# Kernel optimization log

Measured on AMD Instinct MI355X. Metric: run time of the kernel, lower is better.

Reference implementation:

```python
import math
import jax, jax.numpy as jnp
import numpy as np

IN_F, OUT_F = 2048, 2048
WINDOW = 64
SPARSE_RATIO = 0.1


def make_block_mask(in_f, out_f, window, ratio, seed=0):
    # Faithful reimplementation of RandomLinear mask construction.
    p0, p1 = min(in_f, out_f), max(in_f, out_f)
    d = math.ceil(p1 / p0)
    x = math.ceil(p0 / window)
    y = math.ceil((p1 // d) / window)
    blocks = x * y
    nnz = math.ceil(blocks * ratio)
    rng = np.random.default_rng(seed)
    ind = rng.permutation(blocks)[:nnz]
    m = np.zeros((p0, p1), np.float32)
    for k in range(nnz):
        bx = int(ind[k]) // y
        by = int(ind[k]) % y
        m[bx * window:(bx + 1) * window, by * window * d:(by + 1) * window * d] = 1.0
    if in_f <= out_f:
        m = m.T  # mask stored as [out_features, in_features]
    return jnp.asarray(m)


def setup_inputs() -> dict:
    key = jax.random.key(0)
    k_x, k_w, k_b = jax.random.split(key, 3)
    x = jax.random.normal(k_x, (4, 8192, IN_F), dtype=jnp.float32)
    mask = make_block_mask(IN_F, OUT_F, WINDOW, SPARSE_RATIO)
    # kaiming_uniform_(a=sqrt(5)) -> U(-bound, bound), bound = sqrt(6/((1+5)*fan_in)) = 1/sqrt(fan_in)
    bound_w = 1.0 / math.sqrt(IN_F)
    weight = jax.random.uniform(k_w, (OUT_F, IN_F), dtype=jnp.float32,
                                minval=-bound_w, maxval=bound_w)
    density = float(jnp.sum(mask)) / (IN_F * OUT_F)
    weight = weight / math.sqrt(density)  # rescale per reset_parameters
    bound_b = 1.0 / math.sqrt(IN_F)
    bias = jax.random.uniform(k_b, (OUT_F,), dtype=jnp.float32,
                              minval=-bound_b, maxval=bound_b)
    return {"input": x, "weight": weight, "mask": mask, "bias": bias}


def reference(input, weight, mask, bias):
    # y = x @ (mask * W)^T + b   ; x: [B,S,in], W/mask: [out,in], b: [out]
    w_eff = mask * weight
    return jnp.einsum('bsi,oi->bso', input, w_eff) + bias
```

## Files before the change

### kernel.cpp

```cpp
#include <hip/hip_runtime.h>

#define IN_F    2048
#define OUT_F   2048
#define BK      64
#define BM      256
#define BN      64
#define NKB     32
#define NOB     32
#define THREADS 256

__global__ __launch_bounds__(THREADS, 2)
void rl_sparse_fp32(const float* __restrict__ x,
                    const float* __restrict__ w,
                    const float* __restrict__ mask,
                    const float* __restrict__ bias,
                    float* __restrict__ out)
{
    __shared__ __align__(16) float xs[BM * BK];
    __shared__ __align__(16) float wsb[BN * BK];

    const int tid = threadIdx.x;
    const int ob  = blockIdx.x & (NOB - 1);
    const int mt  = blockIdx.x >> 5;
    const size_t m_base = (size_t)mt * BM;
    const int n_base = ob * BN;

    const int lane = tid & 63;
    float mv = 0.0f;
    if (lane < NKB)
        mv = mask[(size_t)n_base * IN_F + (size_t)lane * BK];
    unsigned long long kbits = __ballot(mv != 0.0f);

    const int tn = tid & 7;
    const int tm = tid >> 3;
    const int selx = tm & 3;
    const int selw = tn & 3;

    const int sc = tid & 15;
    const int sr = tid >> 4;

    float acc[8][8];
    #pragma unroll
    for (int i = 0; i < 8; ++i)
        #pragma unroll
        for (int j = 0; j < 8; ++j) acc[i][j] = 0.0f;

    while (kbits) {
        const int kb = __ffsll(kbits) - 1;
        kbits &= (kbits - 1);
        const size_t kcol = (size_t)kb * BK;

        const float* xg = x + m_base * IN_F + kcol + sc * 4;
        float4 vx[BM / 16];
        #pragma unroll
        for (int it = 0; it < BM / 16; ++it)
            vx[it] = *(const float4*)(xg + (size_t)(sr + 16 * it) * IN_F);

        const float* wg = w    + (size_t)(n_base + sr) * IN_F + kcol + sc * 4;
        const float* mg = mask + (size_t)(n_base + sr) * IN_F + kcol + sc * 4;
        float4 vw[BN / 16];
        #pragma unroll
        for (int it = 0; it < BN / 16; ++it) {
            float4 a = *(const float4*)(wg + (size_t)(16 * it) * IN_F);
            float4 b = *(const float4*)(mg + (size_t)(16 * it) * IN_F);
            a.x *= b.x; a.y *= b.y; a.z *= b.z; a.w *= b.w;
            vw[it] = a;
        }

        __syncthreads();

        #pragma unroll
        for (int it = 0; it < BM / 16; ++it) {
            const int r = sr + 16 * it;
            const int ch = sc ^ ((r >> 3) & 3);
            *(float4*)(&xs[r * BK + ch * 4]) = vx[it];
        }
        #pragma unroll
        for (int it = 0; it < BN / 16; ++it) {
            const int r = sr + 16 * it;
            const int ch = sc ^ ((r >> 3) & 3);
            *(float4*)(&wsb[r * BK + ch * 4]) = vw[it];
        }
        __syncthreads();

        const float* xrow = &xs[tm * 8 * BK];
        const float* wrow = &wsb[tn * 8 * BK];
        #pragma unroll 4
        for (int kc = 0; kc < 16; ++kc) {
            const int offx = ((kc ^ selx) << 2);
            const int offw = ((kc ^ selw) << 2);
            float4 xv[8], wv[8];
            #pragma unroll
            for (int i = 0; i < 8; ++i)
                xv[i] = *(const float4*)(xrow + i * BK + offx);
            #pragma unroll
            for (int j = 0; j < 8; ++j)
                wv[j] = *(const float4*)(wrow + j * BK + offw);
            #pragma unroll
            for (int i = 0; i < 8; ++i)
                #pragma unroll
                for (int j = 0; j < 8; ++j) {
                    acc[i][j] += xv[i].x * wv[j].x;
                    acc[i][j] += xv[i].y * wv[j].y;
                    acc[i][j] += xv[i].z * wv[j].z;
                    acc[i][j] += xv[i].w * wv[j].w;
                }
        }
    }

    const float4 b0 = *(const float4*)(bias + n_base + tn * 8);
    const float4 b1 = *(const float4*)(bias + n_base + tn * 8 + 4);
    #pragma unroll
    for (int i = 0; i < 8; ++i) {
        const size_t row = m_base + tm * 8 + i;
        float* op = out + row * OUT_F + n_base + tn * 8;
        float4 o0 = make_float4(acc[i][0] + b0.x, acc[i][1] + b0.y,
                                acc[i][2] + b0.z, acc[i][3] + b0.w);
        float4 o1 = make_float4(acc[i][4] + b1.x, acc[i][5] + b1.y,
                                acc[i][6] + b1.z, acc[i][7] + b1.w);
        *(float4*)(op)     = o0;
        *(float4*)(op + 4) = o1;
    }
}

extern "C" void kernel_launch(void* const* d_in, const int* in_sizes, int n_in,
                              void* d_out, int out_size, void* d_ws, size_t ws_size,
                              hipStream_t stream) {
    const float* x    = (const float*)d_in[0];
    const float* w    = (const float*)d_in[1];
    const float* mask = (const float*)d_in[2];
    const float* bias = (const float*)d_in[3];
    float* out = (float*)d_out;

    const int M = in_sizes[0] / IN_F;
    dim3 grid((M / BM) * NOB);
    rl_sparse_fp32<<<grid, THREADS, 0, stream>>>(x, w, mask, bias, out);
}
```

Before: 1.202 ms.

## Stream x tiles into LDS with global_load_lds and halve K-stage size

Splits each 64-wide K block into two 32-wide stages and loads x directly from global memory into LDS with the AMD global_load_lds builtin, using an XOR swizzle so no register staging is needed. Weight and mask loads for the next stage are prefetched into registers while the current stage computes. The smaller LDS footprint lets occupancy rise to three blocks per CU. The output column mapping changes to split columns into two 32-wide halves. The cost is twice as many barriers per K block and correctness that depends on the swizzle and on the direct-to-LDS write layout.

New measurement: 1.372 ms. +14.1%, slower.

```diff
diff --git a/kernel.cpp b/kernel.cpp
--- a/kernel.cpp
+++ b/kernel.cpp
@@ -2,22 +2,26 @@
 
 #define IN_F    2048
 #define OUT_F   2048
-#define BK      64
+#define BKW     64
+#define BSTAGE  32
 #define BM      256
 #define BN      64
 #define NKB     32
 #define NOB     32
 #define THREADS 256
 
-__global__ __launch_bounds__(THREADS, 2)
-void rl_sparse_fp32(const float* __restrict__ x,
-                    const float* __restrict__ w,
-                    const float* __restrict__ mask,
-                    const float* __restrict__ bias,
-                    float* __restrict__ out)
+typedef __attribute__((address_space(3))) void lds_void_t;
+typedef const __attribute__((address_space(1))) void gbl_void_t;
+
+__global__ __launch_bounds__(THREADS, 3)
+void rl_sparse_v2(const float* __restrict__ x,
+                  const float* __restrict__ w,
+                  const float* __restrict__ mask,
+                  const float* __restrict__ bias,
+                  float* __restrict__ out)
 {
-    __shared__ __align__(16) float xs[BM * BK];
-    __shared__ __align__(16) float wsb[BN * BK];
+    __shared__ __align__(16) float xs[BM * BSTAGE];
+    __shared__ __align__(16) float wsb[BN * BSTAGE];
 
     const int tid = threadIdx.x;
     const int ob  = blockIdx.x & (NOB - 1);
@@ -26,18 +30,19 @@
     const int n_base = ob * BN;
 
     const int lane = tid & 63;
-    float mv = 0.0f;
-    if (lane < NKB)
-        mv = mask[(size_t)n_base * IN_F + (size_t)lane * BK];
-    unsigned long long kbits = __ballot(mv != 0.0f);
+    float mvs = 0.0f;
+    if (lane < NKB) mvs = mask[(size_t)n_base * IN_F + (size_t)lane * BKW];
+    unsigned long long rem = __ballot(mvs != 0.0f);
 
     const int tn = tid & 7;
     const int tm = tid >> 3;
-    const int selx = tm & 3;
-    const int selw = tn & 3;
 
-    const int sc = tid & 15;
-    const int sr = tid >> 4;
+    const int gl_wave = tid >> 6;
+    const int gl_l    = tid & 63;
+
+    const int wrow = tid >> 2;
+    const int wc0  = tid & 3;
+    const int selw_st = (wrow >> 2) & 7;
 
     float acc[8][8];
     #pragma unroll
@@ -45,57 +50,77 @@
         #pragma unroll
         for (int j = 0; j < 8; ++j) acc[i][j] = 0.0f;
 
-    while (kbits) {
-        const int kb = __ffsll(kbits) - 1;
-        kbits &= (kbits - 1);
-        const size_t kcol = (size_t)kb * BK;
+    int cur_kb = rem ? (__ffsll(rem) - 1) : -1;
+    int cur_half = 0;
 
-        const float* xg = x + m_base * IN_F + kcol + sc * 4;
-        float4 vx[BM / 16];
-        #pragma unroll
-        for (int it = 0; it < BM / 16; ++it)
-            vx[it] = *(const float4*)(xg + (size_t)(sr + 16 * it) * IN_F);
+    float4 wra, wrb, mra, mrb;
+    if (cur_kb >= 0) {
+        const size_t kc0 = (size_t)cur_kb * BKW;
+        const float* wp = w    + (size_t)(n_base + wrow) * IN_F + kc0;
+        const float* mp = mask + (size_t)(n_base + wrow) * IN_F + kc0;
+        wra = *(const float4*)(wp + wc0 * 4);
+        wrb = *(const float4*)(wp + (wc0 + 4) * 4);
+        mra = *(const float4*)(mp + wc0 * 4);
+        mrb = *(const float4*)(mp + (wc0 + 4) * 4);
+    }
 
-        const float* wg = w    + (size_t)(n_base + sr) * IN_F + kcol + sc * 4;
-        const float* mg = mask + (size_t)(n_base + sr) * IN_F + kcol + sc * 4;
-        float4 vw[BN / 16];
-        #pragma unroll
-        for (int it = 0; it < BN / 16; ++it) {
-            float4 a = *(const float4*)(wg + (size_t)(16 * it) * IN_F);
-            float4 b = *(const float4*)(mg + (size_t)(16 * it) * IN_F);
-            a.x *= b.x; a.y *= b.y; a.z *= b.z; a.w *= b.w;
-            vw[it] = a;
+    while (cur_kb >= 0) {
+        const size_t kcol = (size_t)cur_kb * BKW + (size_t)cur_half * BSTAGE;
+
+        unsigned long long nrem = rem;
+        int nxt_kb = cur_kb, nxt_half = cur_half + 1;
+        if (nxt_half == 2) {
+            nrem &= (nrem - 1);
+            nxt_half = 0;
+            nxt_kb = nrem ? (__ffsll(nrem) - 1) : -1;
         }
 
         __syncthreads();
 
         #pragma unroll
-        for (int it = 0; it < BM / 16; ++it) {
-            const int r = sr + 16 * it;
-            const int ch = sc ^ ((r >> 3) & 3);
-            *(float4*)(&xs[r * BK + ch * 4]) = vx[it];
+        for (int I = 0; I < 8; ++I) {
+            const int row = gl_wave * 64 + I * 8 + (gl_l >> 3);
+            const int cch = (gl_l & 7) ^ I;
+            const float* src = x + (m_base + row) * (size_t)IN_F + kcol + cch * 4;
+            __builtin_amdgcn_global_load_lds((gbl_void_t*)src,
+                                             (lds_void_t*)&xs[(gl_wave * 64 + I * 8) * BSTAGE],
+                                             16, 0, 0);
         }
-        #pragma unroll
-        for (int it = 0; it < BN / 16; ++it) {
-            const int r = sr + 16 * it;
-            const int ch = sc ^ ((r >> 3) & 3);
-            *(float4*)(&wsb[r * BK + ch * 4]) = vw[it];
+
+        float4 va, vb;
+        va.x = wra.x * mra.x; va.y = wra.y * mra.y; va.z = wra.z * mra.z; va.w = wra.w * mra.w;
+        vb.x = wrb.x * mrb.x; vb.y = wrb.y * mrb.y; vb.z = wrb.z * mrb.z; vb.w = wrb.w * mrb.w;
+
+        if (nxt_kb >= 0) {
+            const size_t nk = (size_t)nxt_kb * BKW + (size_t)nxt_half * BSTAGE;
+            const float* wp = w    + (size_t)(n_base + wrow) * IN_F + nk;
+            const float* mp = mask + (size_t)(n_base + wrow) * IN_F + nk;
+            wra = *(const float4*)(wp + wc0 * 4);
+            wrb = *(const float4*)(wp + (wc0 + 4) * 4);
+            mra = *(const float4*)(mp + wc0 * 4);
+            mrb = *(const float4*)(mp + (wc0 + 4) * 4);
         }
+
+        *(float4*)(&wsb[wrow * BSTAGE + ((wc0 ^ selw_st) << 2)])       = va;
+        *(float4*)(&wsb[wrow * BSTAGE + (((wc0 + 4) ^ selw_st) << 2)]) = vb;
+
         __syncthreads();
 
-        const float* xrow = &xs[tm * 8 * BK];
-        const float* wrow = &wsb[tn * 8 * BK];
+        const float* xrow = &xs[tm * 8 * BSTAGE];
         #pragma unroll 4
-        for (int kc = 0; kc < 16; ++kc) {
-            const int offx = ((kc ^ selx) << 2);
-            const int offw = ((kc ^ selw) << 2);
+        for (int kc = 0; kc < 8; ++kc) {
+            const int offx = ((kc ^ (tm & 7)) << 2);
+            const int offw = ((kc ^ tn) << 2);
             float4 xv[8], wv[8];
             #pragma unroll
             for (int i = 0; i < 8; ++i)
-                xv[i] = *(const float4*)(xrow + i * BK + offx);
+                xv[i] = *(const float4*)(xrow + i * BSTAGE + offx);
             #pragma unroll
-            for (int j = 0; j < 8; ++j)
-                wv[j] = *(const float4*)(wrow + j * BK + offw);
+            for (int j = 0; j < 4; ++j)
+                wv[j] = *(const float4*)(&wsb[(tn * 4 + j) * BSTAGE + offw]);
+            #pragma unroll
+            for (int j = 0; j < 4; ++j)
+                wv[4 + j] = *(const float4*)(&wsb[(32 + tn * 4 + j) * BSTAGE + offw]);
             #pragma unroll
             for (int i = 0; i < 8; ++i)
                 #pragma unroll
@@ -106,20 +131,22 @@
                     acc[i][j] += xv[i].w * wv[j].w;
                 }
         }
+
+        cur_kb = nxt_kb; cur_half = nxt_half; rem = nrem;
     }
 
-    const float4 b0 = *(const float4*)(bias + n_base + tn * 8);
-    const float4 b1 = *(const float4*)(bias + n_base + tn * 8 + 4);
+    const float4 b0 = *(const float4*)(bias + n_base + tn * 4);
+    const float4 b1 = *(const float4*)(bias + n_base + 32 + tn * 4);
     #pragma unroll
     for (int i = 0; i < 8; ++i) {
         const size_t row = m_base + tm * 8 + i;
-        float* op = out + row * OUT_F + n_base + tn * 8;
+        float* op = out + row * OUT_F + n_base;
         float4 o0 = make_float4(acc[i][0] + b0.x, acc[i][1] + b0.y,
                                 acc[i][2] + b0.z, acc[i][3] + b0.w);
         float4 o1 = make_float4(acc[i][4] + b1.x, acc[i][5] + b1.y,
                                 acc[i][6] + b1.z, acc[i][7] + b1.w);
-        *(float4*)(op)     = o0;
-        *(float4*)(op + 4) = o1;
+        *(float4*)(op + tn * 4)      = o0;
+        *(float4*)(op + 32 + tn * 4) = o1;
     }
 }
 
@@ -134,5 +161,5 @@
 
     const int M = in_sizes[0] / IN_F;
     dim3 grid((M / BM) * NOB);
-    rl_sparse_fp32<<<grid, THREADS, 0, stream>>>(x, w, mask, bias, out);
+    rl_sparse_v2<<<grid, THREADS, 0, stream>>>(x, w, mask, bias, out);
 }
```
